# Kernel tuning notes

Hardware: AMD Instinct MI355X
Metric: run time of the kernel (lower is better)

Reference implementation:

```python
import jax, jax.numpy as jnp
import numpy as np

N_NODES = 50000
N_EDGES = 1_600_000
D = 128


def setup_inputs() -> dict:
    key = jax.random.key(0)
    ks = jax.random.split(key, 8)
    s = 1.0 / np.sqrt(D)
    return {
        "x": jax.random.normal(ks[0], (N_NODES, D), dtype=jnp.float32),
        "edge_index": jax.random.randint(ks[1], (2, N_EDGES), 0, N_NODES, dtype=jnp.int64),
        "W1l": jax.random.normal(ks[2], (D, D), dtype=jnp.float32) * s,
        "b1": jnp.zeros((D,), dtype=jnp.float32),
        "W1r": jax.random.normal(ks[3], (D, D), dtype=jnp.float32) * s,
        "W2l": jax.random.normal(ks[4], (D, D), dtype=jnp.float32) * s,
        "b2": jnp.zeros((D,), dtype=jnp.float32),
        "W2r": jax.random.normal(ks[5], (D, D), dtype=jnp.float32) * s,
    }


def _sage_conv(x, src, dst, Wl, b, Wr, num_nodes):
    # mean-aggregate source features at destination nodes
    msg = x[src]                                              # [E, d] gather
    summed = jax.ops.segment_sum(msg, dst, num_segments=num_nodes)
    cnt = jax.ops.segment_sum(jnp.ones((src.shape[0], 1), x.dtype), dst,
                              num_segments=num_nodes)
    mean = summed / jnp.maximum(cnt, 1.0)                     # clamp like PyG
    return mean @ Wl.T + b + x @ Wr.T


def reference(x, edge_index, W1l, b1, W1r, W2l, b2, W2r):
    src, dst = edge_index[0], edge_index[1]
    n = x.shape[0]
    h = _sage_conv(x, src, dst, W1l, b1, W1r, n)
    h = jax.nn.relu(h)
    out = _sage_conv(h, src, dst, W2l, b2, W2r, n)
    return out
```

## Files before the change

### kernel.cpp

```cpp
#include <hip/hip_runtime.h>

#define NN 50000
#define NE 1600000
#define DD 128

#define L1T 512
#define VPT 4
#define EPB (L1T * VPT)
#define NB1 ((NE + EPB - 1) / EPB)
#define NBUCK ((NN + 127) >> 7)
#define BSTRIDE 5120

typedef __attribute__((ext_vector_type(8))) short bf16x8;
typedef __attribute__((ext_vector_type(4))) float f32x4;
typedef __attribute__((ext_vector_type(2))) float f32x2;

__device__ __forceinline__ ushort f2b(float f) {
    unsigned u = __float_as_uint(f);
    return (ushort)((u + 0x7FFFu + ((u >> 16) & 1u)) >> 16);
}


__global__ __launch_bounds__(256) void prep_kernel(const float* __restrict__ x,
                                                   unsigned* __restrict__ xq,
                                                   const float* __restrict__ W1l,
                                                   const float* __restrict__ W1r,
                                                   const float* __restrict__ W2l,
                                                   const float* __restrict__ W2r,
                                                   ushort* __restrict__ Wsw1,
                                                   ushort* __restrict__ Wsw2,
                                                   int* __restrict__ g_fill) {
    int b = blockIdx.x, tid = threadIdx.x;
    if (b < 6250) {
        int i = b * 256 + tid;
        float4 v = ((const float4*)x)[i];
        int w = __builtin_amdgcn_cvt_pk_fp8_f32(v.x, v.y, 0, false);
        w = __builtin_amdgcn_cvt_pk_fp8_f32(v.z, v.w, w, true);
        xq[i] = (unsigned)w;
    } else if (b < 6506) {
        int idx = (b - 6250) * 256 + tid;
        int which = idx >> 15, r = idx & 32767;
        int c = r >> 8, k = r & 255;
        const float* Wl = which ? W2l : W1l;
        const float* Wr = which ? W2r : W1r;
        ushort* Wsw = which ? Wsw2 : Wsw1;
        float v = (k < 128) ? Wl[c * 128 + k] : Wr[c * 128 + (k - 128)];
        Wsw[((k >> 5) * 128 + c) * 32 + (k & 31)] = f2b(v);
    } else {
        for (int i = tid; i < 512; i += 256) g_fill[i] = 0;
    }
}


__global__ __launch_bounds__(L1T) void l1_scatter(const int* __restrict__ src,
                                                  const int* __restrict__ dst,
                                                  int* __restrict__ g_fill,
                                                  unsigned* __restrict__ l1out) {
    __shared__ int lhist[L1T];
    __shared__ int lscan[L1T];
    __shared__ int lrsv[L1T];
    __shared__ int lfill[L1T];
    __shared__ unsigned staged[EPB];
    int tid = threadIdx.x;
    lhist[tid] = 0;
    lfill[tid] = 0;
    __syncthreads();

    unsigned myv[VPT];
    int base = blockIdx.x * EPB;
#pragma unroll
    for (int i = 0; i < VPT; ++i) {
        int idx = base + i * L1T + tid;
        if (idx < NE) {
            unsigned d = (unsigned)dst[idx], s = (unsigned)src[idx];
            myv[i] = (d << 16) | s;
            atomicAdd(&lhist[d >> 7], 1);
        } else {
            myv[i] = 0xFFFFFFFFu;
        }
    }
    __syncthreads();

    lscan[tid] = lhist[tid];
    __syncthreads();
    for (int off = 1; off < L1T; off <<= 1) {
        int t = (tid >= off) ? lscan[tid - off] : 0;
        __syncthreads();
        lscan[tid] += t;
        __syncthreads();
    }

    int cntb = lhist[tid];
    if (cntb > 0) lrsv[tid] = atomicAdd(&g_fill[tid], cntb);

#pragma unroll
    for (int i = 0; i < VPT; ++i) {
        unsigned v = myv[i];
        if (v != 0xFFFFFFFFu) {
            int b = (v >> 16) >> 7;
            int p = lscan[b] - lhist[b] + atomicAdd(&lfill[b], 1);
            staged[p] = v;
        }
    }
    __syncthreads();

    int n = lscan[L1T - 1];
    for (int i = tid; i < n; i += L1T) {
        unsigned v = staged[i];
        int b = (v >> 16) >> 7;
        int g = lrsv[b] + (i - (lscan[b] - lhist[b]));
        if (g < BSTRIDE) l1out[(size_t)b * BSTRIDE + g] = v;
    }
}


__global__ __launch_bounds__(1024) void l2_kernel(const int* __restrict__ g_fill,
                                                  const unsigned* __restrict__ l1out,
                                                  unsigned short* __restrict__ su,
                                                  int* __restrict__ rp) {
    int B = blockIdx.x;
    int tid = threadIdx.x;
    __shared__ int gsc[512];
    __shared__ int h2[1024], sc[1024], f2[1024];
    if (tid < 512) gsc[tid] = (tid < NBUCK) ? g_fill[tid] : 0;
    __syncthreads();
    for (int off = 1; off < 512; off <<= 1) {
        int t = (tid >= off && tid < 512) ? gsc[tid - off] : 0;
        __syncthreads();
        if (tid < 512) gsc[tid] += t;
        __syncthreads();
    }
    int base = gsc[B] - g_fill[B];
    int cnt = g_fill[B];
    if (cnt > BSTRIDE) cnt = BSTRIDE;
    h2[tid] = 0;
    f2[tid] = 0;
    __syncthreads();
    const unsigned* in = l1out + (size_t)B * BSTRIDE;
    for (int i = tid; i < cnt; i += 1024) {
        unsigned v = in[i];
        int key = (int)((v >> 16) & 127) * 8 + (int)((v & 0xFFFFu) >> 13);
        atomicAdd(&h2[key], 1);
    }
    __syncthreads();
    sc[tid] = h2[tid];
    __syncthreads();
    for (int off = 1; off < 1024; off <<= 1) {
        int t = (tid >= off) ? sc[tid - off] : 0;
        __syncthreads();
        sc[tid] += t;
        __syncthreads();
    }
    if ((tid & 7) == 0) {
        int n = B * 128 + (tid >> 3);
        if (n < NN) rp[n] = base + sc[tid] - h2[tid];
    }
    if (B == 0 && tid == 0) rp[NN] = NE;
    __syncthreads();
    for (int i = tid; i < cnt; i += 1024) {
        unsigned v = in[i];
        int key = (int)((v >> 16) & 127) * 8 + (int)((v & 0xFFFFu) >> 13);
        int p = atomicAdd(&f2[key], 1);
        su[base + sc[key] - h2[key] + p] = (unsigned short)(v & 0xFFFFu);
    }
}


#define ADD8(V) { f32x2 t_;                                                         \
    t_ = __builtin_amdgcn_cvt_pk_f32_fp8(V.x, false); acc[0] += t_.x; acc[1] += t_.y; \
    t_ = __builtin_amdgcn_cvt_pk_f32_fp8(V.x, true);  acc[2] += t_.x; acc[3] += t_.y; \
    t_ = __builtin_amdgcn_cvt_pk_f32_fp8(V.y, false); acc[4] += t_.x; acc[5] += t_.y; \
    t_ = __builtin_amdgcn_cvt_pk_f32_fp8(V.y, true);  acc[6] += t_.x; acc[7] += t_.y; }

__global__ __launch_bounds__(256) void agg_fp8(const unsigned char* __restrict__ xq,
                                               const int* __restrict__ rp,
                                               const unsigned short* __restrict__ su,
                                               ushort* __restrict__ meanb) {
    int wave = threadIdx.x >> 6, lane = threadIdx.x & 63;
    int node = blockIdx.x * 4 + wave;
    if (node >= NN) return;
    int start = __builtin_amdgcn_readfirstlane(rp[node]);
    int end   = __builtin_amdgcn_readfirstlane(rp[node + 1]);
    int eslot = lane >> 4, chunk = lane & 15;
    float acc[8] = {};
    int e = start + eslot;
    for (; e + 12 < end; e += 16) {
        unsigned s0 = su[e], s1 = su[e + 4], s2 = su[e + 8], s3 = su[e + 12];
        uint2 v0 = *(const uint2*)(xq + (size_t)s0 * 128 + chunk * 8);
        uint2 v1 = *(const uint2*)(xq + (size_t)s1 * 128 + chunk * 8);
        uint2 v2 = *(const uint2*)(xq + (size_t)s2 * 128 + chunk * 8);
        uint2 v3 = *(const uint2*)(xq + (size_t)s3 * 128 + chunk * 8);
        ADD8(v0); ADD8(v1); ADD8(v2); ADD8(v3);
    }
    for (; e < end; e += 4) {
        unsigned s0 = su[e];
        uint2 v0 = *(const uint2*)(xq + (size_t)s0 * 128 + chunk * 8);
        ADD8(v0);
    }
#pragma unroll
    for (int j = 0; j < 8; ++j) {
        acc[j] += __shfl_xor(acc[j], 16, 64);
        acc[j] += __shfl_xor(acc[j], 32, 64);
    }
    if (eslot == 0) {
        int cnt = end - start;
        float inv = 1.0f / (float)(cnt > 1 ? cnt : 1);
        uint4 o;
        o.x = (unsigned)f2b(acc[0] * inv) | ((unsigned)f2b(acc[1] * inv) << 16);
        o.y = (unsigned)f2b(acc[2] * inv) | ((unsigned)f2b(acc[3] * inv) << 16);
        o.z = (unsigned)f2b(acc[4] * inv) | ((unsigned)f2b(acc[5] * inv) << 16);
        o.w = (unsigned)f2b(acc[6] * inv) | ((unsigned)f2b(acc[7] * inv) << 16);
        *(uint4*)(meanb + (size_t)node * DD + chunk * 8) = o;
    }
}


template <int L1>
__global__ __launch_bounds__(256) void gemm_mfma(const ushort* __restrict__ meanb,
                                                 const float* __restrict__ xf,
                                                 const ushort* __restrict__ ah,
                                                 const ushort* __restrict__ Wsw,
                                                 const float* __restrict__ bias,
                                                 float* __restrict__ outf,
                                                 ushort* __restrict__ outh,
                                                 unsigned char* __restrict__ outq) {
    __shared__ __align__(16) ushort WbL[8][128][32];
    int tid = threadIdx.x;
    int wave = tid >> 6, lane = tid & 63;
    int wave_r = wave >> 1, wave_c = wave & 1;
    int r0 = blockIdx.x * 32 + wave_r * 16;
    int c0 = wave_c * 64;
    int arow = r0 + (lane & 15);
    if (arow >= NN) arow = NN - 1;
    int kg = (lane >> 4) * 8;
    int c = lane & 15;

    bf16x8 af[8];
#pragma unroll
    for (int kc = 0; kc < 4; ++kc)
        af[kc] = *(const bf16x8*)(meanb + (size_t)arow * 128 + kc * 32 + kg);
#pragma unroll
    for (int kc = 4; kc < 8; ++kc) {
        if (L1) {
            const float* ap = xf + (size_t)arow * 128 + (kc - 4) * 32 + kg;
            float4 a = *(const float4*)ap;
            float4 b = *(const float4*)(ap + 4);
            bf16x8 v;
            v[0] = (short)f2b(a.x); v[1] = (short)f2b(a.y);
            v[2] = (short)f2b(a.z); v[3] = (short)f2b(a.w);
            v[4] = (short)f2b(b.x); v[5] = (short)f2b(b.y);
            v[6] = (short)f2b(b.z); v[7] = (short)f2b(b.w);
            af[kc] = v;
        } else {
            af[kc] = *(const bf16x8*)(ah + (size_t)arow * 128 + (kc - 4) * 32 + kg);
        }
    }

    {
        const uint4* Wg = (const uint4*)Wsw;
        uint4* Wl4 = (uint4*)&WbL[0][0][0];
#pragma unroll
        for (int it = 0; it < 16; ++it) {
            int idx = it * 256 + tid;
            Wl4[idx] = Wg[idx];
        }
    }
    __syncthreads();

    f32x4 acc[4] = {};
#pragma unroll
    for (int kc = 0; kc < 8; ++kc) {
#pragma unroll
        for (int t = 0; t < 4; ++t) {
            bf16x8 bf = *(const bf16x8*)&WbL[kc][c0 + t * 16 + c][kg];
            acc[t] = __builtin_amdgcn_mfma_f32_16x16x32_bf16(af[kc], bf, acc[t], 0, 0, 0);
        }
    }

    int rbase = r0 + (lane >> 4) * 4;
#pragma unroll
    for (int t = 0; t < 4; ++t) {
        float bj = bias[c0 + t * 16 + c];
#pragma unroll
        for (int i = 0; i < 4; ++i) {
            int r = rbase + i;
            if (r < NN) {
                float v = acc[t][i] + bj;
                if (L1) {
                    v = fmaxf(v, 0.f);
                    outh[(size_t)r * 128 + c0 + t * 16 + c] = f2b(v);
                    int q = __builtin_amdgcn_cvt_pk_fp8_f32(v, v, 0, false);
                    outq[(size_t)r * 128 + c0 + t * 16 + c] = (unsigned char)q;
                } else {
                    outf[(size_t)r * 128 + c0 + t * 16 + c] = v;
                }
            }
        }
    }
}


extern "C" void kernel_launch(void* const* d_in, const int* in_sizes, int n_in,
                              void* d_out, int out_size, void* d_ws, size_t ws_size,
                              hipStream_t stream) {
    const float* x   = (const float*)d_in[0];
    const int*   ei  = (const int*)d_in[1];
    const float* W1l = (const float*)d_in[2];
    const float* b1  = (const float*)d_in[3];
    const float* W1r = (const float*)d_in[4];
    const float* W2l = (const float*)d_in[5];
    const float* b2  = (const float*)d_in[6];
    const float* W2r = (const float*)d_in[7];
    float* out = (float*)d_out;

    const int* src = ei;
    const int* dst = ei + NE;

    char* ws = (char*)d_ws;
    size_t off = 0;
    auto carve = [&](size_t bytes) {
        char* p = ws + off;
        off = (off + bytes + 255) & ~(size_t)255;
        return p;
    };
    int*            rp     = (int*)carve((NN + 1) * sizeof(int));
    int*            g_fill = (int*)carve(512 * sizeof(int));
    unsigned short* su     = (unsigned short*)carve((size_t)NE * sizeof(unsigned short));
    unsigned*       xq     = (unsigned*)carve((size_t)NN * DD);
    unsigned char*  hq     = (unsigned char*)carve((size_t)NN * DD);
    ushort*         meanb  = (ushort*)carve((size_t)NN * DD * sizeof(ushort));
    ushort*         hh     = (ushort*)carve((size_t)NN * DD * sizeof(ushort));
    ushort*         Wsw1   = (ushort*)carve(128 * 256 * sizeof(ushort));
    ushort*         Wsw2   = (ushort*)carve(128 * 256 * sizeof(ushort));
    unsigned*       l1out  = (unsigned*)hh;

    prep_kernel<<<6507, 256, 0, stream>>>(x, xq, W1l, W1r, W2l, W2r, Wsw1, Wsw2, g_fill);
    l1_scatter<<<NB1, L1T, 0, stream>>>(src, dst, g_fill, l1out);
    l2_kernel<<<NBUCK, 1024, 0, stream>>>(g_fill, l1out, su, rp);

    const int GBLK = (NN + 31) / 32;

    agg_fp8<<<(NN + 3) / 4, 256, 0, stream>>>((const unsigned char*)xq, rp, su, meanb);
    gemm_mfma<1><<<GBLK, 256, 0, stream>>>(meanb, x, nullptr, Wsw1, b1, nullptr, hh, hq);

    agg_fp8<<<(NN + 3) / 4, 256, 0, stream>>>(hq, rp, su, meanb);
    gemm_mfma<0><<<GBLK, 256, 0, stream>>>(meanb, nullptr, hh, Wsw2, b2, out, nullptr, nullptr);
}
```

Baseline: 157.8 us.

## Fuse prep into scatter, use wave-shuffle scans, persistent GEMM grid

Folds the x-to-fp8 quantization and weight swizzle into the l1_scatter kernel and replaces the g_fill-zeroing block with a hipMemsetAsync, which removes one kernel launch. The shared-memory Hillis-Steele scans in l1_scatter and l2_kernel become wave-level __shfl_up scans followed by a small cross-wave scan, cutting the number of __syncthreads barriers. The GEMM kernels now run as a persistent grid of 512 blocks that loops over row tiles, so each block loads the 64KB weight tile into shared memory once instead of once per tile. The costs are extra work in the scatter blocks and less parallelism in the GEMM.

```diff
diff --git a/kernel.cpp b/kernel.cpp
--- a/kernel.cpp
+++ b/kernel.cpp
@@ -10,6 +10,8 @@
 #define NB1 ((NE + EPB - 1) / EPB)
 #define NBUCK ((NN + 127) >> 7)
 #define BSTRIDE 5120
+#define GBLK ((NN + 31) / 32)
+#define GGRID 512
 
 typedef __attribute__((ext_vector_type(8))) short bf16x8;
 typedef __attribute__((ext_vector_type(4))) float f32x4;
@@ -21,47 +23,47 @@
 }
 
 
-__global__ __launch_bounds__(256) void prep_kernel(const float* __restrict__ x,
-                                                   unsigned* __restrict__ xq,
-                                                   const float* __restrict__ W1l,
-                                                   const float* __restrict__ W1r,
-                                                   const float* __restrict__ W2l,
-                                                   const float* __restrict__ W2r,
-                                                   ushort* __restrict__ Wsw1,
-                                                   ushort* __restrict__ Wsw2,
-                                                   int* __restrict__ g_fill) {
-    int b = blockIdx.x, tid = threadIdx.x;
-    if (b < 6250) {
-        int i = b * 256 + tid;
-        float4 v = ((const float4*)x)[i];
-        int w = __builtin_amdgcn_cvt_pk_fp8_f32(v.x, v.y, 0, false);
-        w = __builtin_amdgcn_cvt_pk_fp8_f32(v.z, v.w, w, true);
-        xq[i] = (unsigned)w;
-    } else if (b < 6506) {
-        int idx = (b - 6250) * 256 + tid;
-        int which = idx >> 15, r = idx & 32767;
+__global__ __launch_bounds__(L1T) void l1_scatter(const int* __restrict__ src,
+                                                  const int* __restrict__ dst,
+                                                  int* __restrict__ g_fill,
+                                                  unsigned* __restrict__ l1out,
+                                                  const float* __restrict__ x,
+                                                  unsigned* __restrict__ xq,
+                                                  const float* __restrict__ W1l,
+                                                  const float* __restrict__ W1r,
+                                                  const float* __restrict__ W2l,
+                                                  const float* __restrict__ W2r,
+                                                  ushort* __restrict__ Wsw1,
+                                                  ushort* __restrict__ Wsw2) {
+    __shared__ int lhist[L1T];
+    __shared__ int lscan[L1T];
+    __shared__ int lrsv[L1T];
+    __shared__ int lfill[L1T];
+    __shared__ int wsum[8];
+    __shared__ unsigned staged[EPB];
+    int tid = threadIdx.x;
+    int gt = blockIdx.x * L1T + tid;
+
+#pragma unroll
+    for (int i = 0; i < 4; ++i) {
+        int idx = gt + i * (NB1 * L1T);
+        if (idx < NN * DD / 4) {
+            float4 v = ((const float4*)x)[idx];
+            int w = __builtin_amdgcn_cvt_pk_fp8_f32(v.x, v.y, 0, false);
+            w = __builtin_amdgcn_cvt_pk_fp8_f32(v.z, v.w, w, true);
+            xq[idx] = (unsigned)w;
+        }
+    }
+    if (gt < 65536) {
+        int which = gt >> 15, r = gt & 32767;
         int c = r >> 8, k = r & 255;
         const float* Wl = which ? W2l : W1l;
         const float* Wr = which ? W2r : W1r;
         ushort* Wsw = which ? Wsw2 : Wsw1;
         float v = (k < 128) ? Wl[c * 128 + k] : Wr[c * 128 + (k - 128)];
         Wsw[((k >> 5) * 128 + c) * 32 + (k & 31)] = f2b(v);
-    } else {
-        for (int i = tid; i < 512; i += 256) g_fill[i] = 0;
-    }
-}
-
-
-__global__ __launch_bounds__(L1T) void l1_scatter(const int* __restrict__ src,
-                                                  const int* __restrict__ dst,
-                                                  int* __restrict__ g_fill,
-                                                  unsigned* __restrict__ l1out) {
-    __shared__ int lhist[L1T];
-    __shared__ int lscan[L1T];
-    __shared__ int lrsv[L1T];
-    __shared__ int lfill[L1T];
-    __shared__ unsigned staged[EPB];
-    int tid = threadIdx.x;
+    }
+
     lhist[tid] = 0;
     lfill[tid] = 0;
     __syncthreads();
@@ -81,14 +83,29 @@
     }
     __syncthreads();
 
-    lscan[tid] = lhist[tid];
-    __syncthreads();
-    for (int off = 1; off < L1T; off <<= 1) {
-        int t = (tid >= off) ? lscan[tid - off] : 0;
+    int lane = tid & 63, wv = tid >> 6;
+    {
+        int sv = lhist[tid];
+#pragma unroll
+        for (int off = 1; off < 64; off <<= 1) {
+            int t = __shfl_up(sv, off, 64);
+            if (lane >= off) sv += t;
+        }
+        if (lane == 63) wsum[wv] = sv;
         __syncthreads();
-        lscan[tid] += t;
+        if (tid < 8) {
+            int w = wsum[tid], sw = w;
+#pragma unroll
+            for (int off = 1; off < 8; off <<= 1) {
+                int t = __shfl_up(sw, off, 64);
+                if (tid >= off) sw += t;
+            }
+            wsum[tid] = sw - w;
+        }
         __syncthreads();
-    }
+        lscan[tid] = sv + wsum[wv];
+    }
+    __syncthreads();
 
     int cntb = lhist[tid];
     if (cntb > 0) lrsv[tid] = atomicAdd(&g_fill[tid], cntb);
@@ -120,22 +137,42 @@
                                                   int* __restrict__ rp) {
     int B = blockIdx.x;
     int tid = threadIdx.x;
+    int lane = tid & 63, wv = tid >> 6;
     __shared__ int gsc[512];
+    __shared__ int ws1[8];
+    __shared__ int ws2[16];
     __shared__ int h2[1024], sc[1024], f2[1024];
-    if (tid < 512) gsc[tid] = (tid < NBUCK) ? g_fill[tid] : 0;
-    __syncthreads();
-    for (int off = 1; off < 512; off <<= 1) {
-        int t = (tid >= off && tid < 512) ? gsc[tid - off] : 0;
-        __syncthreads();
-        if (tid < 512) gsc[tid] += t;
-        __syncthreads();
-    }
+
+    int gsv = 0;
+    if (tid < 512) {
+        gsv = (tid < NBUCK) ? g_fill[tid] : 0;
+#pragma unroll
+        for (int off = 1; off < 64; off <<= 1) {
+            int t = __shfl_up(gsv, off, 64);
+            if (lane >= off) gsv += t;
+        }
+        if (lane == 63) ws1[wv] = gsv;
+    }
+    h2[tid] = 0;
+    f2[tid] = 0;
+    __syncthreads();
+    if (tid < 8) {
+        int w = ws1[tid], sw = w;
+#pragma unroll
+        for (int off = 1; off < 8; off <<= 1) {
+            int t = __shfl_up(sw, off, 64);
+            if (tid >= off) sw += t;
+        }
+        ws1[tid] = sw - w;
+    }
+    __syncthreads();
+    if (tid < 512) gsc[tid] = gsv + ws1[wv];
+    __syncthreads();
+
     int base = gsc[B] - g_fill[B];
     int cnt = g_fill[B];
     if (cnt > BSTRIDE) cnt = BSTRIDE;
-    h2[tid] = 0;
-    f2[tid] = 0;
-    __syncthreads();
+
     const unsigned* in = l1out + (size_t)B * BSTRIDE;
     for (int i = tid; i < cnt; i += 1024) {
         unsigned v = in[i];
@@ -143,14 +180,30 @@
         atomicAdd(&h2[key], 1);
     }
     __syncthreads();
-    sc[tid] = h2[tid];
-    __syncthreads();
-    for (int off = 1; off < 1024; off <<= 1) {
-        int t = (tid >= off) ? sc[tid - off] : 0;
+
+    {
+        int sv = h2[tid];
+#pragma unroll
+        for (int off = 1; off < 64; off <<= 1) {
+            int t = __shfl_up(sv, off, 64);
+            if (lane >= off) sv += t;
+        }
+        if (lane == 63) ws2[wv] = sv;
         __syncthreads();
-        sc[tid] += t;
+        if (tid < 16) {
+            int w = ws2[tid], sw = w;
+#pragma unroll
+            for (int off = 1; off < 16; off <<= 1) {
+                int t = __shfl_up(sw, off, 64);
+                if (tid >= off) sw += t;
+            }
+            ws2[tid] = sw - w;
+        }
         __syncthreads();
-    }
+        sc[tid] = sv + ws2[wv];
+    }
+    __syncthreads();
+
     if ((tid & 7) == 0) {
         int n = B * 128 + (tid >> 3);
         if (n < NN) rp[n] = base + sc[tid] - h2[tid];
@@ -228,71 +281,73 @@
     int tid = threadIdx.x;
     int wave = tid >> 6, lane = tid & 63;
     int wave_r = wave >> 1, wave_c = wave & 1;
-    int r0 = blockIdx.x * 32 + wave_r * 16;
     int c0 = wave_c * 64;
-    int arow = r0 + (lane & 15);
-    if (arow >= NN) arow = NN - 1;
     int kg = (lane >> 4) * 8;
     int c = lane & 15;
-
-    bf16x8 af[8];
-#pragma unroll
-    for (int kc = 0; kc < 4; ++kc)
-        af[kc] = *(const bf16x8*)(meanb + (size_t)arow * 128 + kc * 32 + kg);
-#pragma unroll
-    for (int kc = 4; kc < 8; ++kc) {
-        if (L1) {
-            const float* ap = xf + (size_t)arow * 128 + (kc - 4) * 32 + kg;
-            float4 a = *(const float4*)ap;
-            float4 b = *(const float4*)(ap + 4);
-            bf16x8 v;
-            v[0] = (short)f2b(a.x); v[1] = (short)f2b(a.y);
-            v[2] = (short)f2b(a.z); v[3] = (short)f2b(a.w);
-            v[4] = (short)f2b(b.x); v[5] = (short)f2b(b.y);
-            v[6] = (short)f2b(b.z); v[7] = (short)f2b(b.w);
-            af[kc] = v;
-        } else {
-            af[kc] = *(const bf16x8*)(ah + (size_t)arow * 128 + (kc - 4) * 32 + kg);
-        }
-    }
 
     {
         const uint4* Wg = (const uint4*)Wsw;
         uint4* Wl4 = (uint4*)&WbL[0][0][0];
 #pragma unroll
-        for (int it = 0; it < 16; ++it) {
-            int idx = it * 256 + tid;
-            Wl4[idx] = Wg[idx];
-        }
-    }
-    __syncthreads();
-
-    f32x4 acc[4] = {};
-#pragma unroll
-    for (int kc = 0; kc < 8; ++kc) {
+        for (int it = 0; it < 16; ++it) Wl4[it * 256 + tid] = Wg[it * 256 + tid];
+    }
+    float bj[4];
+#pragma unroll
+    for (int t = 0; t < 4; ++t) bj[t] = bias[c0 + t * 16 + c];
+    __syncthreads();
+
+    for (int tile = blockIdx.x; tile < GBLK; tile += GGRID) {
+        int r0 = tile * 32 + wave_r * 16;
+        int arow = r0 + (lane & 15);
+        if (arow >= NN) arow = NN - 1;
+
+        bf16x8 af[8];
+#pragma unroll
+        for (int kc = 0; kc < 4; ++kc)
+            af[kc] = *(const bf16x8*)(meanb + (size_t)arow * 128 + kc * 32 + kg);
+#pragma unroll
+        for (int kc = 4; kc < 8; ++kc) {
+            if (L1) {
+                const float* ap = xf + (size_t)arow * 128 + (kc - 4) * 32 + kg;
+                float4 a = *(const float4*)ap;
+                float4 b = *(const float4*)(ap + 4);
+                bf16x8 v;
+                v[0] = (short)f2b(a.x); v[1] = (short)f2b(a.y);
+                v[2] = (short)f2b(a.z); v[3] = (short)f2b(a.w);
+                v[4] = (short)f2b(b.x); v[5] = (short)f2b(b.y);
+                v[6] = (short)f2b(b.z); v[7] = (short)f2b(b.w);
+                af[kc] = v;
+            } else {
+                af[kc] = *(const bf16x8*)(ah + (size_t)arow * 128 + (kc - 4) * 32 + kg);
+            }
+        }
+
+        f32x4 acc[4] = {};
+#pragma unroll
+        for (int kc = 0; kc < 8; ++kc) {
+#pragma unroll
+            for (int t = 0; t < 4; ++t) {
+                bf16x8 bf = *(const bf16x8*)&WbL[kc][c0 + t * 16 + c][kg];
+                acc[t] = __builtin_amdgcn_mfma_f32_16x16x32_bf16(af[kc], bf, acc[t], 0, 0, 0);
+            }
+        }
+
+        int rbase = r0 + (lane >> 4) * 4;
 #pragma unroll
         for (int t = 0; t < 4; ++t) {
-            bf16x8 bf = *(const bf16x8*)&WbL[kc][c0 + t * 16 + c][kg];
-            acc[t] = __builtin_amdgcn_mfma_f32_16x16x32_bf16(af[kc], bf, acc[t], 0, 0, 0);
-        }
-    }
-
-    int rbase = r0 + (lane >> 4) * 4;
-#pragma unroll
-    for (int t = 0; t < 4; ++t) {
-        float bj = bias[c0 + t * 16 + c];
-#pragma unroll
-        for (int i = 0; i < 4; ++i) {
-            int r = rbase + i;
-            if (r < NN) {
-                float v = acc[t][i] + bj;
-                if (L1) {
-                    v = fmaxf(v, 0.f);
-                    outh[(size_t)r * 128 + c0 + t * 16 + c] = f2b(v);
-                    int q = __builtin_amdgcn_cvt_pk_fp8_f32(v, v, 0, false);
-                    outq[(size_t)r * 128 + c0 + t * 16 + c] = (unsigned char)q;
-                } else {
-                    outf[(size_t)r * 128 + c0 + t * 16 + c] = v;
+#pragma unroll
+            for (int i = 0; i < 4; ++i) {
+                int r = rbase + i;
+                if (r < NN) {
+                    float v = acc[t][i] + bj[t];
+                    if (L1) {
+                        v = fmaxf(v, 0.f);
+                        outh[(size_t)r * 128 + c0 + t * 16 + c] = f2b(v);
+                        int q = __builtin_amdgcn_cvt_pk_fp8_f32(v, v, 0, false);
+                        outq[(size_t)r * 128 + c0 + t * 16 + c] = (unsigned char)q;
+                    } else {
+                        outf[(size_t)r * 128 + c0 + t * 16 + c] = v;
+                    }
                 }
             }
         }
@@ -334,15 +389,15 @@
     ushort*         Wsw2   = (ushort*)carve(128 * 256 * sizeof(ushort));
     unsigned*       l1out  = (unsigned*)hh;
 
-    prep_kernel<<<6507, 256, 0, stream>>>(x, xq, W1l, W1r, W2l, W2r, Wsw1, Wsw2, g_fill);
-    l1_scatter<<<NB1, L1T, 0, stream>>>(src, dst, g_fill, l1out);
+    hipMemsetAsync(g_fill, 0, 512 * sizeof(int), stream);
+
+    l1_scatter<<<NB1, L1T, 0, stream>>>(src, dst, g_fill, l1out,
+                                        x, xq, W1l, W1r, W2l, W2r, Wsw1, Wsw2);
     l2_kernel<<<NBUCK, 1024, 0, stream>>>(g_fill, l1out, su, rp);
 
-    const int GBLK = (NN + 31) / 32;
-
     agg_fp8<<<(NN + 3) / 4, 256, 0, stream>>>((const unsigned char*)xq, rp, su, meanb);
-    gemm_mfma<1><<<GBLK, 256, 0, stream>>>(meanb, x, nullptr, Wsw1, b1, nullptr, hh, hq);
+    gemm_mfma<1><<<GGRID, 256, 0, stream>>>(meanb, x, nullptr, Wsw1, b1, nullptr, hh, hq);
 
     agg_fp8<<<(NN + 3) / 4, 256, 0, stream>>>(hq, rp, su, meanb);
-    gemm_mfma<0><<<GBLK, 256, 0, stream>>>(meanb, nullptr, hh, Wsw2, b2, out, nullptr, nullptr);
-}
+    gemm_mfma<0><<<GGRID, 256, 0, stream>>>(meanb, nullptr, hh, Wsw2, b2, out, nullptr, nullptr);
+}
```

Result: faster. 140.7 us (-10.8%).
